# Optimization experiments

Measured on AMD Instinct MI355X. Metric: run time of the kernel, lower is better.

## Reference

```python
import jax, jax.numpy as jnp
import numpy as np

N = 100000        # nodes
E = 1600000       # edges (N * avg_degree 16)
D_IN = 128
D_OUT = 32
OBS_T = 60        # observation_time -> decay table size 60*OBS_T = 3600
T_MAX = 60 * OBS_T


def setup_inputs() -> dict:
    key = jax.random.key(0)
    ks = jax.random.split(key, 8)
    inp = {
        "input": jax.random.normal(ks[0], (N, D_IN), dtype=jnp.float32),
        "W": jax.random.normal(ks[1], (D_IN, D_OUT), dtype=jnp.float32) * (np.sqrt(2.0) / np.sqrt(D_IN)),
        # decay weights are abs(normal(0, 0.02)) in the original; rand*0.04 is same scale
        "decay_weight1": jnp.abs(jax.random.normal(ks[2], (T_MAX, 1), dtype=jnp.float32) * 0.02),
        "decay_weight2": jnp.abs(jax.random.normal(ks[3], (T_MAX, 1), dtype=jnp.float32) * 0.02),
        "edge_row": jax.random.randint(ks[4], (E,), 0, N, dtype=jnp.int32),
        "edge_col": jax.random.randint(ks[5], (E,), 0, N, dtype=jnp.int32),
        # zero-based interval index; equals (adj_value - 1) of the original code
        "edge_time": jax.random.randint(ks[6], (E,), 0, T_MAX, dtype=jnp.int32),
        "arrive_time": jax.random.randint(ks[7], (N,), 0, T_MAX, dtype=jnp.int32),
        "observation_time": OBS_T,
    }
    return inp


def reference(input, W, decay_weight1, decay_weight2,
              edge_row, edge_col, edge_time, arrive_time, observation_time):
    n_nodes = input.shape[0]
    # h = relu(input @ W)  [N, D_OUT]
    h = jax.nn.relu(jnp.matmul(input, W))
    # one-hot(interval) @ decay_weight1 == embedding lookup  -> per-edge decay scalar
    decay = decay_weight1[edge_time, 0]                        # [E]
    # SpecialSpmm: out[i] = sum_{edges (i,j)} decay_e * h[j]  (gather-scale-scatter)
    msgs = decay[:, None] * h[edge_col]                        # [E, D_OUT]
    h_prime = jax.ops.segment_sum(msgs, edge_row, num_segments=n_nodes)
    # outlayer window decay: one-hot(60*T - arrive - 1) @ decay_weight2 == lookup
    win_idx = 60 * observation_time - arrive_time - 1          # [N] in [0, 60*T)
    h_prime = decay_weight2[win_idx, 0][:, None] * h_prime
    return h_prime
```

## Files before the change

### kernel.cpp

```cpp
#include <hip/hip_runtime.h>

#define N_NODES 100000
#define N_EDGES 1600000
#define D_IN    128
#define D_OUT   32
#define CROWS   2048
#define NCB     49
#define NSH     8
#define NSEG    (NCB * NSH)
#define CAP_A   4500
#define DEPTH   48
#define SEGSTRIDE 4608
#define SSTRIDE 2064
#define CAPW    1024
#define RPB3    32
#define K3_BLKS (NCB * 64)
#define GEMM_BLKS ((N_NODES + 63) / 64)
#define GRID_A  2048
#define EPB_A   ((N_EDGES + GRID_A - 1) / GRID_A)

typedef __attribute__((ext_vector_type(8))) short bf16x8;
typedef __attribute__((ext_vector_type(4))) float f32x4;

__device__ inline short f2bf(float f) {
    union { float f; unsigned u; } v; v.f = f;
    unsigned r = (v.u + 0x7FFFu + ((v.u >> 16) & 1u)) >> 16;
    return (short)r;
}

union SMemGA {
    struct { short wbt[D_IN * D_OUT]; } g;
    struct { uint2 lbin[NCB][DEPTH]; int lcnt[NCB]; int gbase[NCB]; } a;
};

__global__ __launch_bounds__(256) void gemm_phaseA_kernel(
    const float* __restrict__ input, const float* __restrict__ W,
    const int* __restrict__ erow,    const int* __restrict__ ecol,
    const int* __restrict__ etime,
    unsigned short* __restrict__ h16,
    int* __restrict__ gcur,
    uint2* __restrict__ segA)
{
    __shared__ SMemGA sm;
    const int tid = threadIdx.x;

    if (blockIdx.x < GEMM_BLKS) {
        for (int i = tid; i < D_IN * D_OUT; i += 256) {
            const int k = i >> 5, c = i & 31;
            sm.g.wbt[c * D_IN + k] = f2bf(W[i]);
        }
        __syncthreads();

        const int wave = tid >> 6;
        const int lane = tid & 63;
        const int r0   = blockIdx.x * 64 + wave * 16;
        const int c16  = lane & 15;
        const int quad = lane >> 4;

        int ra = r0 + c16;
        if (ra >= N_NODES) ra = N_NODES - 1;
        const float* arow = input + (size_t)ra * D_IN;

        f32x4 acc0 = {0.f, 0.f, 0.f, 0.f};
        f32x4 acc1 = {0.f, 0.f, 0.f, 0.f};
#pragma unroll
        for (int q = 0; q < 4; ++q) {
            const float* ap = arow + q * 32 + quad * 8;
            f32x4 a0 = *(const f32x4*)(ap);
            f32x4 a1 = *(const f32x4*)(ap + 4);
            bf16x8 af;
            af[0] = f2bf(a0.x); af[1] = f2bf(a0.y); af[2] = f2bf(a0.z); af[3] = f2bf(a0.w);
            af[4] = f2bf(a1.x); af[5] = f2bf(a1.y); af[6] = f2bf(a1.z); af[7] = f2bf(a1.w);
            bf16x8 b0 = *(const bf16x8*)(sm.g.wbt + (c16)      * D_IN + q * 32 + quad * 8);
            bf16x8 b1 = *(const bf16x8*)(sm.g.wbt + (c16 + 16) * D_IN + q * 32 + quad * 8);
            acc0 = __builtin_amdgcn_mfma_f32_16x16x32_bf16(af, b0, acc0, 0, 0, 0);
            acc1 = __builtin_amdgcn_mfma_f32_16x16x32_bf16(af, b1, acc1, 0, 0, 0);
        }
#pragma unroll
        for (int i = 0; i < 4; ++i) {
            const int rr = r0 + quad * 4 + i;
            if (rr < N_NODES) {
                h16[(size_t)rr * D_OUT + c16]      = (unsigned short)f2bf(fmaxf(acc0[i], 0.f));
                h16[(size_t)rr * D_OUT + c16 + 16] = (unsigned short)f2bf(fmaxf(acc1[i], 0.f));
            }
        }
    } else {
        const int blk   = blockIdx.x - GEMM_BLKS;
        const int shard = blk & (NSH - 1);
        const int wv    = tid >> 6;
        const int ln    = tid & 63;

        if (tid < NCB) sm.a.lcnt[tid] = 0;
        __syncthreads();

        const int e_beg = blk * EPB_A;
        const int e_end = min(e_beg + EPB_A, N_EDGES);

        for (int e = e_beg + tid; e < e_end; e += 256) {
            const int row = erow[e];
            const int cb  = row >> 11;
            uint2 p;
            p.x = (unsigned)ecol[e] | ((unsigned)(row & (CROWS - 1)) << 17);
            p.y = (unsigned)etime[e];
            const int pos = atomicAdd(&sm.a.lcnt[cb], 1);
            if (pos < DEPTH) sm.a.lbin[cb][pos] = p;
            else {
                const int gp = atomicAdd(&gcur[(cb * NSH + shard) * 16], 1);
                if (gp < CAP_A) segA[(size_t)(cb * NSH + shard) * CAP_A + gp] = p;
            }
        }
        __syncthreads();

        if (tid < NCB) {
            const int c = min(sm.a.lcnt[tid], DEPTH);
            sm.a.gbase[tid] = atomicAdd(&gcur[(tid * NSH + shard) * 16], c);
        }
        __syncthreads();

        for (int bin = wv; bin < NCB; bin += 4) {
            const int c  = min(sm.a.lcnt[bin], DEPTH);
            const int gb = sm.a.gbase[bin];
            uint2* seg = segA + (size_t)(bin * NSH + shard) * CAP_A;
            for (int k = ln; k < c; k += 64)
                if (gb + k < CAP_A) seg[gb + k] = sm.a.lbin[bin][k];
        }
    }
}

__global__ __launch_bounds__(256) void sortseg_kernel(
    const int* __restrict__ gcur, const uint2* __restrict__ segA,
    int* __restrict__ sseg, unsigned* __restrict__ spk2s)
{
    __shared__ int hist[CROWS];
    __shared__ int curs[CROWS];
    __shared__ int part[256];

    const int b   = blockIdx.x;
    const int tid = threadIdx.x;
    const int n   = min(gcur[b * 16], CAP_A);
    const uint2* seg = segA + (size_t)b * CAP_A;

    for (int t = tid; t < CROWS; t += 256) hist[t] = 0;
    __syncthreads();

    for (int i = tid; i < n; i += 256)
        atomicAdd(&hist[(seg[i].x >> 17) & (CROWS - 1)], 1);
    __syncthreads();

    int tmp[8]; int s0 = 0;
    const int base = tid * 8;
#pragma unroll
    for (int k = 0; k < 8; ++k) { tmp[k] = hist[base + k]; s0 += tmp[k]; }
    part[tid] = s0;
    __syncthreads();
    for (int off = 1; off < 256; off <<= 1) {
        int v = part[tid];
        if (tid >= off) v += part[tid - off];
        __syncthreads(); part[tid] = v; __syncthreads();
    }
    int run = part[tid] - s0;
#pragma unroll
    for (int k = 0; k < 8; ++k) { curs[base + k] = run; run += tmp[k]; }
    __syncthreads();

    int* sg = sseg + (size_t)b * SSTRIDE;
    for (int t = tid; t < CROWS; t += 256) sg[t] = curs[t];
    if (tid == 0) sg[CROWS] = n;
    __syncthreads();

    unsigned* dst = spk2s + (size_t)b * SEGSTRIDE;
    for (int i = tid; i < n; i += 256) {
        const uint2 p  = seg[i];
        const int   rl = (p.x >> 17) & (CROWS - 1);
        dst[atomicAdd(&curs[rl], 1)] = (p.x & 0x1FFFFu) | (p.y << 20);
    }
}

__global__ __launch_bounds__(256) void merge_reduce_kernel(
    const unsigned short* __restrict__ h16, const int* __restrict__ sseg,
    const unsigned* __restrict__ spk2s,
    const float* __restrict__ dw1, const float* __restrict__ dw2,
    const int* __restrict__ arrive, const int* __restrict__ obs,
    float* __restrict__ out)
{
    __shared__ int ls8[NSH][RPB3 + 1];
    __shared__ int pre[NSH][RPB3];
    __shared__ int totL[RPB3];
    __shared__ int dstart[RPB3 + 1];
    __shared__ unsigned st[CAPW];

    const int b   = blockIdx.x;
    const int cb  = b >> 6;
    const int rl0 = (b & 63) * RPB3;
    const int g0  = cb * CROWS + rl0;
    if (g0 >= N_NODES) return;
    const int tid = threadIdx.x;

    for (int t = tid; t < NSH * (RPB3 + 1); t += 256) {
        const int s = t / (RPB3 + 1), i = t - s * (RPB3 + 1);
        ls8[s][i] = sseg[(size_t)(cb * NSH + s) * SSTRIDE + rl0 + i];
    }
    __syncthreads();

    if (tid < RPB3) {
        int accp = 0;
#pragma unroll
        for (int s = 0; s < NSH; ++s) {
            pre[s][tid] = accp;
            accp += ls8[s][tid + 1] - ls8[s][tid];
        }
        totL[tid] = accp;
    }
    __syncthreads();
    if (tid == 0) {
        int runp = 0;
#pragma unroll
        for (int r = 0; r < RPB3; ++r) { dstart[r] = runp; runp += totL[r]; }
        dstart[RPB3] = runp;
    }
    __syncthreads();

#pragma unroll
    for (int s = 0; s < NSH; ++s) {
        const int sb   = ls8[s][0];
        const int span = ls8[s][RPB3] - sb;
        const unsigned* src = spk2s + (size_t)(cb * NSH + s) * SEGSTRIDE;
        for (int i = tid; i < span; i += 256) {
            const int gidx = sb + i;
            int lo = 0, hi = RPB3 - 1;
#pragma unroll
            for (int it = 0; it < 5; ++it) {
                const int mid = (lo + hi + 1) >> 1;
                if (ls8[s][mid] <= gidx) lo = mid; else hi = mid - 1;
            }
            const int pos = dstart[lo] + pre[s][lo] + (gidx - ls8[s][lo]);
            if (pos < CAPW) st[pos] = src[gidx];
        }
    }
    __syncthreads();

    const int g  = tid >> 3;
    const int li = tid & 7;
    const int row = g0 + g;
    const int begc = min(dstart[g], CAPW);
    const int endc = min(dstart[g + 1], CAPW);
    const int n    = endc - begc;
    const unsigned* recs = &st[begc];
    const unsigned short* hp = h16 + li * 4;

    float a0 = 0.f, a1 = 0.f, a2 = 0.f, a3 = 0.f;
    int j = 0;
    for (; j + 8 <= n; j += 8) {
#pragma unroll
        for (int u = 0; u < 8; ++u) {
            const unsigned rec = recs[j + u];
            const uint2 hv = *(const uint2*)(hp + ((size_t)(rec & 0x1FFFFu) << 5));
            const float w  = dw1[rec >> 20];
            a0 = fmaf(w, __uint_as_float(hv.x << 16),         a0);
            a1 = fmaf(w, __uint_as_float(hv.x & 0xFFFF0000u), a1);
            a2 = fmaf(w, __uint_as_float(hv.y << 16),         a2);
            a3 = fmaf(w, __uint_as_float(hv.y & 0xFFFF0000u), a3);
        }
    }
    for (; j < n; ++j) {
        const unsigned rec = recs[j];
        const uint2 hv = *(const uint2*)(hp + ((size_t)(rec & 0x1FFFFu) << 5));
        const float w  = dw1[rec >> 20];
        a0 = fmaf(w, __uint_as_float(hv.x << 16),         a0);
        a1 = fmaf(w, __uint_as_float(hv.x & 0xFFFF0000u), a1);
        a2 = fmaf(w, __uint_as_float(hv.y << 16),         a2);
        a3 = fmaf(w, __uint_as_float(hv.y & 0xFFFF0000u), a3);
    }

    const int T = 60 * obs[0];
    const float sdw = dw2[T - arrive[row] - 1];
    float4 o;
    o.x = a0 * sdw; o.y = a1 * sdw; o.z = a2 * sdw; o.w = a3 * sdw;
    *(float4*)(out + ((size_t)row << 5) + li * 4) = o;
}

extern "C" void kernel_launch(void* const* d_in, const int* in_sizes, int n_in,
                              void* d_out, int out_size, void* d_ws, size_t ws_size,
                              hipStream_t stream)
{
    const float* input  = (const float*)d_in[0];
    const float* W      = (const float*)d_in[1];
    const float* dw1    = (const float*)d_in[2];
    const float* dw2    = (const float*)d_in[3];
    const int*   erow   = (const int*)d_in[4];
    const int*   ecol   = (const int*)d_in[5];
    const int*   etime  = (const int*)d_in[6];
    const int*   arrive = (const int*)d_in[7];
    const int*   obs    = (const int*)d_in[8];

    float* out = (float*)d_out;

    char* p = (char*)d_ws;
    unsigned short* h16 = (unsigned short*)p;
    p += (size_t)N_NODES * D_OUT * 2;
    p = (char*)(((size_t)p + 255) & ~(size_t)255);
    int* gcur = (int*)p;
    p += (size_t)NSEG * 16 * 4;
    p = (char*)(((size_t)p + 255) & ~(size_t)255);
    uint2* segA = (uint2*)p;
    p += (size_t)NSEG * CAP_A * 8;
    p = (char*)(((size_t)p + 255) & ~(size_t)255);
    unsigned* spk2s = (unsigned*)p;
    p += (size_t)NSEG * SEGSTRIDE * 4;
    p = (char*)(((size_t)p + 255) & ~(size_t)255);
    int* sseg = (int*)p;

    hipMemsetAsync(gcur, 0, (size_t)NSEG * 16 * 4, stream);

    gemm_phaseA_kernel<<<GEMM_BLKS + GRID_A, 256, 0, stream>>>(
        input, W, erow, ecol, etime, h16, gcur, segA);
    sortseg_kernel<<<NSEG, 256, 0, stream>>>(gcur, segA, sseg, spk2s);
    merge_reduce_kernel<<<K3_BLKS, 256, 0, stream>>>(
        h16, sseg, spk2s, dw1, dw2, arrive, obs, out);
}
```

Baseline: 181.4 us.

## Move GEMM blocks from the binning kernel into the segment-sort kernel

The dense relu(input@W) GEMM blocks are moved out of the edge-binning kernel and co-scheduled with the per-segment counting sort instead. The binning kernel becomes edge-only. The small 392-block sort launch now shares the GPU with the 1563 GEMM blocks, so the latency-bound sort can overlap with bandwidth-bound GEMM work. Sort blocks come first in the grid so they start early, but the shared-memory union grows to the sort's footprint, which may lower GEMM occupancy.

```diff
diff --git a/kernel.cpp b/kernel.cpp
--- a/kernel.cpp
+++ b/kernel.cpp
@@ -28,23 +28,111 @@
     return (short)r;
 }
 
-union SMemGA {
-    struct { short wbt[D_IN * D_OUT]; } g;
-    struct { uint2 lbin[NCB][DEPTH]; int lcnt[NCB]; int gbase[NCB]; } a;
-};
-
-__global__ __launch_bounds__(256) void gemm_phaseA_kernel(
-    const float* __restrict__ input, const float* __restrict__ W,
+__global__ __launch_bounds__(256) void phaseA_kernel(
     const int* __restrict__ erow,    const int* __restrict__ ecol,
     const int* __restrict__ etime,
-    unsigned short* __restrict__ h16,
     int* __restrict__ gcur,
     uint2* __restrict__ segA)
 {
-    __shared__ SMemGA sm;
+    __shared__ struct { uint2 lbin[NCB][DEPTH]; int lcnt[NCB]; int gbase[NCB]; } sm;
     const int tid = threadIdx.x;
 
-    if (blockIdx.x < GEMM_BLKS) {
+    const int blk   = blockIdx.x;
+    const int shard = blk & (NSH - 1);
+    const int wv    = tid >> 6;
+    const int ln    = tid & 63;
+
+    if (tid < NCB) sm.lcnt[tid] = 0;
+    __syncthreads();
+
+    const int e_beg = blk * EPB_A;
+    const int e_end = min(e_beg + EPB_A, N_EDGES);
+
+    for (int e = e_beg + tid; e < e_end; e += 256) {
+        const int row = erow[e];
+        const int cb  = row >> 11;
+        uint2 p;
+        p.x = (unsigned)ecol[e] | ((unsigned)(row & (CROWS - 1)) << 17);
+        p.y = (unsigned)etime[e];
+        const int pos = atomicAdd(&sm.lcnt[cb], 1);
+        if (pos < DEPTH) sm.lbin[cb][pos] = p;
+        else {
+            const int gp = atomicAdd(&gcur[(cb * NSH + shard) * 16], 1);
+            if (gp < CAP_A) segA[(size_t)(cb * NSH + shard) * CAP_A + gp] = p;
+        }
+    }
+    __syncthreads();
+
+    if (tid < NCB) {
+        const int c = min(sm.lcnt[tid], DEPTH);
+        sm.gbase[tid] = atomicAdd(&gcur[(tid * NSH + shard) * 16], c);
+    }
+    __syncthreads();
+
+    for (int bin = wv; bin < NCB; bin += 4) {
+        const int c  = min(sm.lcnt[bin], DEPTH);
+        const int gb = sm.gbase[bin];
+        uint2* seg = segA + (size_t)(bin * NSH + shard) * CAP_A;
+        for (int k = ln; k < c; k += 64)
+            if (gb + k < CAP_A) seg[gb + k] = sm.lbin[bin][k];
+    }
+}
+
+union SMemGS {
+    struct { short wbt[D_IN * D_OUT]; } g;
+    struct { int hist[CROWS]; int curs[CROWS]; int part[256]; } s;
+};
+
+__global__ __launch_bounds__(256) void gemm_sortseg_kernel(
+    const float* __restrict__ input, const float* __restrict__ W,
+    unsigned short* __restrict__ h16,
+    const int* __restrict__ gcur, const uint2* __restrict__ segA,
+    int* __restrict__ sseg, unsigned* __restrict__ spk2s)
+{
+    __shared__ SMemGS sm;
+    const int tid = threadIdx.x;
+
+    if (blockIdx.x < NSEG) {
+        const int b = blockIdx.x;
+        const int n = min(gcur[b * 16], CAP_A);
+        const uint2* seg = segA + (size_t)b * CAP_A;
+
+        for (int t = tid; t < CROWS; t += 256) sm.s.hist[t] = 0;
+        __syncthreads();
+
+        for (int i = tid; i < n; i += 256)
+            atomicAdd(&sm.s.hist[(seg[i].x >> 17) & (CROWS - 1)], 1);
+        __syncthreads();
+
+        int tmp[8]; int s0 = 0;
+        const int base = tid * 8;
+#pragma unroll
+        for (int k = 0; k < 8; ++k) { tmp[k] = sm.s.hist[base + k]; s0 += tmp[k]; }
+        sm.s.part[tid] = s0;
+        __syncthreads();
+        for (int off = 1; off < 256; off <<= 1) {
+            int v = sm.s.part[tid];
+            if (tid >= off) v += sm.s.part[tid - off];
+            __syncthreads(); sm.s.part[tid] = v; __syncthreads();
+        }
+        int run = sm.s.part[tid] - s0;
+#pragma unroll
+        for (int k = 0; k < 8; ++k) { sm.s.curs[base + k] = run; run += tmp[k]; }
+        __syncthreads();
+
+        int* sg = sseg + (size_t)b * SSTRIDE;
+        for (int t = tid; t < CROWS; t += 256) sg[t] = sm.s.curs[t];
+        if (tid == 0) sg[CROWS] = n;
+        __syncthreads();
+
+        unsigned* dst = spk2s + (size_t)b * SEGSTRIDE;
+        for (int i = tid; i < n; i += 256) {
+            const uint2 p  = seg[i];
+            const int   rl = (p.x >> 17) & (CROWS - 1);
+            dst[atomicAdd(&sm.s.curs[rl], 1)] = (p.x & 0x1FFFFu) | (p.y << 20);
+        }
+    } else {
+        const int gblk = blockIdx.x - NSEG;
         for (int i = tid; i < D_IN * D_OUT; i += 256) {
             const int k = i >> 5, c = i & 31;
             sm.g.wbt[c * D_IN + k] = f2bf(W[i]);
@@ -53,7 +141,7 @@
 
         const int wave = tid >> 6;
         const int lane = tid & 63;
-        const int r0   = blockIdx.x * 64 + wave * 16;
+        const int r0   = gblk * 64 + wave * 16;
         const int c16  = lane & 15;
         const int quad = lane >> 4;
 
@@ -84,95 +172,6 @@
                 h16[(size_t)rr * D_OUT + c16 + 16] = (unsigned short)f2bf(fmaxf(acc1[i], 0.f));
             }
         }
-    } else {
-        const int blk   = blockIdx.x - GEMM_BLKS;
-        const int shard = blk & (NSH - 1);
-        const int wv    = tid >> 6;
-        const int ln    = tid & 63;
-
-        if (tid < NCB) sm.a.lcnt[tid] = 0;
-        __syncthreads();
-
-        const int e_beg = blk * EPB_A;
-        const int e_end = min(e_beg + EPB_A, N_EDGES);
-
-        for (int e = e_beg + tid; e < e_end; e += 256) {
-            const int row = erow[e];
-            const int cb  = row >> 11;
-            uint2 p;
-            p.x = (unsigned)ecol[e] | ((unsigned)(row & (CROWS - 1)) << 17);
-            p.y = (unsigned)etime[e];
-            const int pos = atomicAdd(&sm.a.lcnt[cb], 1);
-            if (pos < DEPTH) sm.a.lbin[cb][pos] = p;
-            else {
-                const int gp = atomicAdd(&gcur[(cb * NSH + shard) * 16], 1);
-                if (gp < CAP_A) segA[(size_t)(cb * NSH + shard) * CAP_A + gp] = p;
-            }
-        }
-        __syncthreads();
-
-        if (tid < NCB) {
-            const int c = min(sm.a.lcnt[tid], DEPTH);
-            sm.a.gbase[tid] = atomicAdd(&gcur[(tid * NSH + shard) * 16], c);
-        }
-        __syncthreads();
-
-        for (int bin = wv; bin < NCB; bin += 4) {
-            const int c  = min(sm.a.lcnt[bin], DEPTH);
-            const int gb = sm.a.gbase[bin];
-            uint2* seg = segA + (size_t)(bin * NSH + shard) * CAP_A;
-            for (int k = ln; k < c; k += 64)
-                if (gb + k < CAP_A) seg[gb + k] = sm.a.lbin[bin][k];
-        }
-    }
-}
-
-__global__ __launch_bounds__(256) void sortseg_kernel(
-    const int* __restrict__ gcur, const uint2* __restrict__ segA,
-    int* __restrict__ sseg, unsigned* __restrict__ spk2s)
-{
-    __shared__ int hist[CROWS];
-    __shared__ int curs[CROWS];
-    __shared__ int part[256];
-
-    const int b   = blockIdx.x;
-    const int tid = threadIdx.x;
-    const int n   = min(gcur[b * 16], CAP_A);
-    const uint2* seg = segA + (size_t)b * CAP_A;
-
-    for (int t = tid; t < CROWS; t += 256) hist[t] = 0;
-    __syncthreads();
-
-    for (int i = tid; i < n; i += 256)
-        atomicAdd(&hist[(seg[i].x >> 17) & (CROWS - 1)], 1);
-    __syncthreads();
-
-    int tmp[8]; int s0 = 0;
-    const int base = tid * 8;
-#pragma unroll
-    for (int k = 0; k < 8; ++k) { tmp[k] = hist[base + k]; s0 += tmp[k]; }
-    part[tid] = s0;
-    __syncthreads();
-    for (int off = 1; off < 256; off <<= 1) {
-        int v = part[tid];
-        if (tid >= off) v += part[tid - off];
-        __syncthreads(); part[tid] = v; __syncthreads();
-    }
-    int run = part[tid] - s0;
-#pragma unroll
-    for (int k = 0; k < 8; ++k) { curs[base + k] = run; run += tmp[k]; }
-    __syncthreads();
-
-    int* sg = sseg + (size_t)b * SSTRIDE;
-    for (int t = tid; t < CROWS; t += 256) sg[t] = curs[t];
-    if (tid == 0) sg[CROWS] = n;
-    __syncthreads();
-
-    unsigned* dst = spk2s + (size_t)b * SEGSTRIDE;
-    for (int i = tid; i < n; i += 256) {
-        const uint2 p  = seg[i];
-        const int   rl = (p.x >> 17) & (CROWS - 1);
-        dst[atomicAdd(&curs[rl], 1)] = (p.x & 0x1FFFFu) | (p.y << 20);
     }
 }
 
@@ -312,9 +311,9 @@
 
     hipMemsetAsync(gcur, 0, (size_t)NSEG * 16 * 4, stream);
 
-    gemm_phaseA_kernel<<<GEMM_BLKS + GRID_A, 256, 0, stream>>>(
-        input, W, erow, ecol, etime, h16, gcur, segA);
-    sortseg_kernel<<<NSEG, 256, 0, stream>>>(gcur, segA, sseg, spk2s);
+    phaseA_kernel<<<GRID_A, 256, 0, stream>>>(erow, ecol, etime, gcur, segA);
+    gemm_sortseg_kernel<<<NSEG + GEMM_BLKS, 256, 0, stream>>>(
+        input, W, h16, gcur, segA, sseg, spk2s);
     merge_reduce_kernel<<<K3_BLKS, 256, 0, stream>>>(
         h16, sseg, spk2s, dw1, dw2, arrive, obs, out);
 }
```

Result: no change. 179.0 us (-1.4%).
